# Kernel optimization log

Hardware: AMD Instinct MI355X
Metric: run time of the kernel (lower is better)

The kernel has to match this reference:

```python
import jax, jax.numpy as jnp
import numpy as np

B, S, D_IN, M, H, F, L, D_OUT = 4, 1024, 256, 1024, 16, 8, 2, 256
HD = M // H
EPS = 1e-5


def setup_inputs() -> dict:
    key = jax.random.key(0)
    ks = iter(jax.random.split(key, 40))
    w = lambda *s: 0.02 * jax.random.normal(next(ks), s, dtype=jnp.float32)
    inp = {
        "x": jax.random.normal(next(ks), (B, S, D_IN), dtype=jnp.float32),
        # phase embedding params
        "Wemb": w(D_IN, M), "bemb": w(M),
        "Wamp": w(M, F), "bamp": w(F),
        "freqs": jnp.logspace(-1, 2, F, dtype=jnp.float32),
        "phase_off": w(F),
        # per-layer attention params, stacked on leading L axis
        "Wq": w(L, M, M), "bq": w(L, M),
        "Wk": w(L, M, M), "bk": w(L, M),
        "Wv": w(L, M, M), "bv": w(L, M),
        "Wo": w(L, M, M), "bo": w(L, M),
        "pbias": w(L, H, F),
        "ln_g": jnp.ones((L, M), dtype=jnp.float32),
        "ln_b": jnp.zeros((L, M), dtype=jnp.float32),
        # output projection MLP
        "W1": w(M, M // 2), "b1": w(M // 2),
        "W2": w(M // 2, D_OUT), "b2": w(D_OUT),
    }
    return inp


def _forward(x, Wemb, bemb, Wamp, bamp, freqs, phase_off,
             Wq, bq, Wk, bk, Wv, bv, Wo, bo, pbias, ln_g, ln_b,
             W1, b1, W2, b2):
    Bsz, Seq, _ = x.shape
    # --- TemporalPhaseEmbedding ---
    m = x @ Wemb + bemb                                   # [B,S,M]
    tc = jnp.arange(Seq, dtype=x.dtype) / Seq * (2.0 * jnp.pi)  # [S]
    amp = jax.nn.softmax(m @ Wamp + bamp, axis=-1)        # [B,S,F]
    pc = tc[:, None] * freqs[None, :] + phase_off         # [S,F] (batch-identical)
    # |m[...,None] * amp * e^{i*pc}| averaged over F == |m| * mean_F(amp)
    pf = jnp.abs(m) * jnp.mean(amp, axis=-1, keepdims=True)  # [B,S,M]
    # phase-coherence, batch-independent since pc is shared across batch
    coh = jnp.cos(pc[:, None, :] - pc[None, :, :])        # [S,S,F]
    scale = 1.0 / jnp.sqrt(jnp.asarray(HD, dtype=x.dtype))
    for l in range(L):
        res = pf
        Q = (pf @ Wq[l] + bq[l]).reshape(Bsz, Seq, H, HD)
        K = (pf @ Wk[l] + bk[l]).reshape(Bsz, Seq, H, HD)
        V = (pf @ Wv[l] + bv[l]).reshape(Bsz, Seq, H, HD)
        bias = jnp.einsum('stf,hf->hst', coh, pbias[l])   # [H,S,S]
        scores = jnp.einsum('bshd,bthd->bhst', Q, K) * scale + bias[None]
        w_attn = jax.nn.softmax(scores, axis=-1)
        att = jnp.einsum('bhst,bthd->bshd', w_attn, V).reshape(Bsz, Seq, M)
        att = att @ Wo[l] + bo[l]
        y = att + res
        mu = jnp.mean(y, axis=-1, keepdims=True)
        var = jnp.var(y, axis=-1, keepdims=True)
        pf = (y - mu) / jnp.sqrt(var + EPS) * ln_g[l] + ln_b[l]
    hdn = jax.nn.relu(pf @ W1 + b1)
    return hdn @ W2 + b2                                  # [B,S,D_OUT]


def reference(x, Wemb, bemb, Wamp, bamp, freqs, phase_off,
              Wq, bq, Wk, bk, Wv, bv, Wo, bo, pbias, ln_g, ln_b,
              W1, b1, W2, b2):
    return _forward(x, Wemb, bemb, Wamp, bamp, freqs, phase_off,
                    Wq, bq, Wk, bk, Wv, bv, Wo, bo, pbias, ln_g, ln_b,
                    W1, b1, W2, b2)
```

## Files before the change

### kernel.cpp

```cpp
#include <hip/hip_runtime.h>
#include <cmath>

#define B_    4
#define S_    1024
#define DIN_  256
#define M_    1024
#define H_    16
#define F_    8
#define L_    2
#define DOUT_ 256
#define NT_   4096

typedef unsigned short u16;
typedef unsigned int   u32;
typedef __bf16 bf16x8 __attribute__((ext_vector_type(8)));
typedef float  f32x4  __attribute__((ext_vector_type(4)));

#define LOG2E 1.4426950408889634f
#define QSCALE (0.125f * LOG2E)

__device__ __forceinline__ u16 f2b(float f) {
    u32 u = __builtin_bit_cast(u32, f);
    u += 0x7fffu + ((u >> 16) & 1u);
    return (u16)(u >> 16);
}
__device__ __forceinline__ float b2f(u32 h) {
    return __builtin_bit_cast(float, h << 16);
}
__device__ __forceinline__ void gload_lds16(const void* g, void* l) {
    __builtin_amdgcn_global_load_lds(
        (const __attribute__((address_space(1))) u32*)g,
        (__attribute__((address_space(3))) u32*)l, 16, 0, 0);
}

__global__ void qcsb_k(const float* __restrict__ freqs,
                       const float* __restrict__ poff,
                       const float* __restrict__ pb,
                       u16* __restrict__ qcs, u16* __restrict__ csb)
{
    const int QN = L_ * H_ * S_ * 16;
    int idx = blockIdx.x * 256 + threadIdx.x;
    if (idx < QN) {
        int f2 = idx & 15, f = f2 & 7;
        int s = (idx >> 4) & 1023;
        int lh = idx >> 14;
        float pc = ((float)s * (6.283185307179586f / 1024.f)) * freqs[f] + poff[f];
        float v = (f2 < 8) ? cosf(pc) : sinf(pc);
        qcs[idx] = f2b(pb[lh * 8 + f] * v * LOG2E);
    } else if (idx < QN + S_ * 16) {
        int i2 = idx - QN;
        int f2 = i2 & 15, f = f2 & 7;
        int s = i2 >> 4;
        float pc = ((float)s * (6.283185307179586f / 1024.f)) * freqs[f] + poff[f];
        csb[i2] = f2b((f2 < 8) ? cosf(pc) : sinf(pc));
    }
}

__global__ void bcat_k(const float* __restrict__ bq, const float* __restrict__ bk,
                       const float* __restrict__ bv, float* __restrict__ bqkv)
{
    int idx = blockIdx.x * 256 + threadIdx.x;
    int l = idx >= 3072;
    int j = idx - l * 3072;
    float v = (j < 1024) ? bq[l * 1024 + j]
            : (j < 2048) ? bk[l * 1024 + j - 1024]
                         : bv[l * 1024 + j - 2048];
    bqkv[idx] = v;
}

__global__ __launch_bounds__(256) void cvt_k(const float* __restrict__ src,
                                             u16* __restrict__ dst)
{
    int i = (blockIdx.x * 256 + threadIdx.x) * 4;
    float4 v = *(const float4*)(src + i);
    *(ushort4*)(dst + i) = make_ushort4(f2b(v.x), f2b(v.y), f2b(v.z), f2b(v.w));
}

__global__ __launch_bounds__(256) void cvtT_k(const float* __restrict__ src,
                                              u16* __restrict__ dst, int K, int N)
{
    __shared__ float t[32][33];
    src += (size_t)blockIdx.z * K * N;
    dst += (size_t)blockIdx.z * K * N;
    const int n0 = blockIdx.x * 32, k0 = blockIdx.y * 32;
    const int r = threadIdx.x >> 3, c4 = (threadIdx.x & 7) << 2;
    float4 v = *(const float4*)(src + (size_t)(k0 + r) * N + n0 + c4);
    t[r][c4 + 0] = v.x; t[r][c4 + 1] = v.y; t[r][c4 + 2] = v.z; t[r][c4 + 3] = v.w;
    __syncthreads();
    ushort4 o = make_ushort4(f2b(t[c4 + 0][r]), f2b(t[c4 + 1][r]),
                             f2b(t[c4 + 2][r]), f2b(t[c4 + 3][r]));
    *(ushort4*)(dst + (size_t)(n0 + r) * K + k0 + c4) = o;
}

__global__ __launch_bounds__(256) void cvtT3_k(const float* __restrict__ Wq,
                                               const float* __restrict__ Wk,
                                               const float* __restrict__ Wv,
                                               u16* __restrict__ dst)
{
    __shared__ float t[32][33];
    const int z = blockIdx.z, l = z / 3, which = z - l * 3;
    const float* src = (which == 0 ? Wq : which == 1 ? Wk : Wv) + (size_t)l * M_ * M_;
    u16* d = dst + (size_t)l * 3072 * 1024 + (size_t)which * 1024 * 1024;
    const int n0 = blockIdx.x * 32, k0 = blockIdx.y * 32;
    const int r = threadIdx.x >> 3, c4 = (threadIdx.x & 7) << 2;
    float4 v = *(const float4*)(src + (size_t)(k0 + r) * 1024 + n0 + c4);
    t[r][c4 + 0] = v.x; t[r][c4 + 1] = v.y; t[r][c4 + 2] = v.z; t[r][c4 + 3] = v.w;
    __syncthreads();
    ushort4 o = make_ushort4(f2b(t[c4 + 0][r]), f2b(t[c4 + 1][r]),
                             f2b(t[c4 + 2][r]), f2b(t[c4 + 3][r]));
    *(ushort4*)(d + (size_t)(n0 + r) * 1024 + k0 + c4) = o;
}

__global__ __launch_bounds__(256) void vT_k(const u16* __restrict__ QKV,
                                            u16* __restrict__ Vt)
{
    __shared__ __attribute__((aligned(16))) u16 Ts[64 * 64];
    const int tid = threadIdx.x;
    const int t0 = blockIdx.x * 64, bh = blockIdx.y;
    const int b = bh >> 4, h = bh & 15;
#pragma unroll
    for (int i = 0; i < 2; ++i) {
        int slot = i * 256 + tid;
        int row = slot >> 3, g8 = slot & 7;
        uint4 v = *(const uint4*)(QKV + (size_t)(b * 1024 + t0 + row) * 3072 + 2048 + h * 64 + g8 * 8);
        int gs = g8 ^ ((row >> 3) & 7);
        *(uint4*)(Ts + row * 64 + gs * 8) = v;
    }
    __syncthreads();
#pragma unroll
    for (int i = 0; i < 2; ++i) {
        int slot = i * 256 + tid;
        int d = slot >> 3, t8 = slot & 7;
        u16 tmp[8];
#pragma unroll
        for (int j = 0; j < 8; ++j) {
            int t = t8 * 8 + j;
            int gd = (d >> 3) ^ ((t >> 3) & 7);
            tmp[j] = Ts[t * 64 + gd * 8 + (d & 7)];
        }
        *(uint4*)(Vt + (size_t)(bh * 64 + d) * 1024 + t0 + t8 * 8) = *(uint4*)tmp;
    }
}

template<int EPI, int OUTBF>
__global__ __launch_bounds__(256, 2) void mgemm_k(
    const u16* __restrict__ A, const u16* __restrict__ Wt,
    const float* __restrict__ bias, void* __restrict__ Cout,
    int N, int K)
{
    __shared__ __attribute__((aligned(16))) u16 As[128 * 64];
    __shared__ __attribute__((aligned(16))) u16 Bs[128 * 64];
    const int tid = threadIdx.x;
    const int lane = tid & 63;
    const int bn = blockIdx.x, bm = blockIdx.y;
    const int wid = tid >> 6, wr = wid >> 1, wc = wid & 1;

    f32x4 acc[4][4];
#pragma unroll
    for (int m = 0; m < 4; ++m)
#pragma unroll
        for (int n = 0; n < 4; ++n) {
            f32x4 z = {0.f, 0.f, 0.f, 0.f};
            acc[m][n] = z;
        }

    const int r = lane & 15, g = lane >> 4;
    const int nk = K >> 6;

    for (int kt = 0; kt < nk; ++kt) {
        const int k0 = kt << 6;
        __syncthreads();
#pragma unroll
        for (int i = 0; i < 4; ++i) {
            int slot = i * 256 + tid;
            int row = slot >> 3;
            int kg = (slot & 7) ^ (row & 7);
            gload_lds16(A + (size_t)(bm * 128 + row) * K + k0 + kg * 8,
                        As + (size_t)(slot & ~63) * 8);
        }
#pragma unroll
        for (int i = 0; i < 4; ++i) {
            int slot = i * 256 + tid;
            int row = slot >> 3;
            int kg = (slot & 7) ^ (row & 7);
            gload_lds16(Wt + (size_t)(bn * 128 + row) * K + k0 + kg * 8,
                        Bs + (size_t)(slot & ~63) * 8);
        }
        __syncthreads();

#pragma unroll
        for (int ks = 0; ks < 2; ++ks) {
            bf16x8 af[4], bfr[4];
#pragma unroll
            for (int m = 0; m < 4; ++m) {
                int row = wr * 64 + m * 16 + r;
                int kg = (ks * 4 + g) ^ (row & 7);
                af[m] = *(const bf16x8*)(As + row * 64 + kg * 8);
            }
#pragma unroll
            for (int n = 0; n < 4; ++n) {
                int row = wc * 64 + n * 16 + r;
                int kg = (ks * 4 + g) ^ (row & 7);
                bfr[n] = *(const bf16x8*)(Bs + row * 64 + kg * 8);
            }
#pragma unroll
            for (int m = 0; m < 4; ++m)
#pragma unroll
                for (int n = 0; n < 4; ++n)
                    acc[m][n] = __builtin_amdgcn_mfma_f32_16x16x32_bf16(
                        af[m], bfr[n], acc[m][n], 0, 0, 0);
        }
    }

#pragma unroll
    for (int n = 0; n < 4; ++n) {
        const int gcol = bn * 128 + wc * 64 + n * 16 + r;
        const float bb = bias[gcol];
#pragma unroll
        for (int m = 0; m < 4; ++m) {
            const int grow0 = bm * 128 + wr * 64 + m * 16 + g * 4;
#pragma unroll
            for (int q = 0; q < 4; ++q) {
                float c = acc[m][n][q] + bb;
                if (EPI == 1) c = fabsf(c) * 0.125f;
                if (EPI == 2) c = fmaxf(c, 0.f);
                if (EPI == 4) c = (gcol < 1024) ? c * QSCALE : c;
                if (OUTBF)
                    ((u16*)Cout)[(size_t)(grow0 + q) * N + gcol] = f2b(c);
                else
                    ((float*)Cout)[(size_t)(grow0 + q) * N + gcol] = c;
            }
        }
    }
}

__global__ __launch_bounds__(512) void fattn_k(
    const u16* __restrict__ QKV, const u16* __restrict__ Vtg,
    const u16* __restrict__ csb, const u16* __restrict__ qcs,
    u16* __restrict__ Og)
{
    __shared__ __attribute__((aligned(16))) u16 Ks2[64 * 64];
    __shared__ __attribute__((aligned(16))) u16 Vt2[64 * 64];
    __shared__ __attribute__((aligned(16))) u16 Ext[64 * 16];
    __shared__ __attribute__((aligned(16))) u16 Pl[8][16 * 68];
    const int tid = threadIdx.x, lane = tid & 63, w = tid >> 6;
    const int c = lane & 15, g = lane >> 4;
    const int h = blockIdx.y, b = blockIdx.z, bh = b * 16 + h;
    const int s0 = blockIdx.x * 128;

    const uint4 zz = {0u, 0u, 0u, 0u};
    const bf16x8 zfrag = __builtin_bit_cast(bf16x8, zz);

    bf16x8 aq[3];
    {
        int sl = s0 + w * 16 + c;
        size_t tok = (size_t)b * 1024 + sl;
        aq[0] = *(const bf16x8*)(QKV + tok * 3072 + h * 64 + g * 8);
        aq[1] = *(const bf16x8*)(QKV + tok * 3072 + h * 64 + 32 + g * 8);
        aq[2] = (g < 2) ? *(const bf16x8*)(qcs + ((size_t)h * 1024 + sl) * 16 + g * 8)
                        : zfrag;
    }

    f32x4 oacc[4];
#pragma unroll
    for (int n = 0; n < 4; ++n) {
        f32x4 z = {0.f, 0.f, 0.f, 0.f};
        oacc[n] = z;
    }
    float lsum = 0.f;

    for (int t0 = 0; t0 < S_; t0 += 64) {
        __syncthreads();
        {
            int row = tid >> 3, gi = tid & 7;
            int kg = (gi ^ (row & 7)) * 8;
            gload_lds16(QKV + (size_t)(b * 1024 + t0 + row) * 3072 + 1024 + h * 64 + kg,
                        Ks2 + (size_t)(tid & ~63) * 8);
            gload_lds16(Vtg + (size_t)(bh * 64 + row) * 1024 + t0 + kg,
                        Vt2 + (size_t)(tid & ~63) * 8);
        }
        if (tid < 128) {
            int row = tid >> 1, gi = tid & 1;
            gload_lds16(csb + (size_t)(t0 + row) * 16 + gi * 8,
                        Ext + (size_t)(tid & ~63) * 8);
        }
        __syncthreads();

        f32x4 sacc[4];
#pragma unroll
        for (int n = 0; n < 4; ++n) {
            f32x4 z = {0.f, 0.f, 0.f, 0.f};
            sacc[n] = z;
        }
#pragma unroll
        for (int ks = 0; ks < 3; ++ks) {
            bf16x8 bk[4];
#pragma unroll
            for (int n = 0; n < 4; ++n) {
                int tr = n * 16 + c;
                if (ks < 2) {
                    int kg = (ks * 4 + g) ^ (tr & 7);
                    bk[n] = *(const bf16x8*)(Ks2 + tr * 64 + kg * 8);
                } else {
                    bk[n] = (g < 2) ? *(const bf16x8*)(Ext + tr * 16 + g * 8) : zfrag;
                }
            }
#pragma unroll
            for (int n = 0; n < 4; ++n)
                sacc[n] = __builtin_amdgcn_mfma_f32_16x16x32_bf16(
                    bk[n], aq[ks], sacc[n], 0, 0, 0);
        }

#pragma unroll
        for (int n = 0; n < 4; ++n) {
            u16 pk[4];
#pragma unroll
            for (int q = 0; q < 4; ++q) {
                float p = __builtin_amdgcn_exp2f(sacc[n][q]);
                lsum += p;
                pk[q] = f2b(p);
            }
            uint2 pv;
            pv.x = (u32)pk[0] | ((u32)pk[1] << 16);
            pv.y = (u32)pk[2] | ((u32)pk[3] << 16);
            *(uint2*)(&Pl[w][c * 68 + n * 16 + g * 4]) = pv;
        }

#pragma unroll
        for (int ks2 = 0; ks2 < 2; ++ks2) {
            bf16x8 pa = *(const bf16x8*)(&Pl[w][c * 68 + ks2 * 32 + g * 8]);
#pragma unroll
            for (int n = 0; n < 4; ++n) {
                int dr = n * 16 + c;
                int kg = (ks2 * 4 + g) ^ (dr & 7);
                bf16x8 vf = *(const bf16x8*)(Vt2 + dr * 64 + kg * 8);
                oacc[n] = __builtin_amdgcn_mfma_f32_16x16x32_bf16(
                    pa, vf, oacc[n], 0, 0, 0);
            }
        }
    }

    float lt = lsum + __shfl_xor(lsum, 16);
    lt += __shfl_xor(lt, 32);
    float inv[4];
#pragma unroll
    for (int q = 0; q < 4; ++q)
        inv[q] = 1.f / __shfl(lt, g * 4 + q);

#pragma unroll
    for (int n = 0; n < 4; ++n)
#pragma unroll
        for (int q = 0; q < 4; ++q) {
            size_t tok = (size_t)b * 1024 + s0 + w * 16 + g * 4 + q;
            Og[tok * 1024 + h * 64 + n * 16 + c] = f2b(oacc[n][q] * inv[q]);
        }
}

__global__ __launch_bounds__(256) void ln_k(
    const u16* __restrict__ Y, u16* __restrict__ Pf,
    const float* __restrict__ g, const float* __restrict__ bt)
{
    const int rw = blockIdx.x;
    const int tid = threadIdx.x;
    const u16* yp = Y + (size_t)rw * M_ + tid * 4;
    u16* pp = Pf + (size_t)rw * M_ + tid * 4;
    ushort4 yv = *(const ushort4*)yp;
    ushort4 rv = *(const ushort4*)pp;
    float a[4];
    a[0] = b2f(yv.x) + b2f(rv.x); a[1] = b2f(yv.y) + b2f(rv.y);
    a[2] = b2f(yv.z) + b2f(rv.z); a[3] = b2f(yv.w) + b2f(rv.w);
    float s = a[0] + a[1] + a[2] + a[3];
    float q = a[0] * a[0] + a[1] * a[1] + a[2] * a[2] + a[3] * a[3];
#pragma unroll
    for (int o = 1; o < 64; o <<= 1) {
        s += __shfl_xor(s, o);
        q += __shfl_xor(q, o);
    }
    __shared__ float ss[4], qq[4];
    if ((tid & 63) == 0) { ss[tid >> 6] = s; qq[tid >> 6] = q; }
    __syncthreads();
    s = ss[0] + ss[1] + ss[2] + ss[3];
    q = qq[0] + qq[1] + qq[2] + qq[3];
    float mu = s * (1.0f / 1024.0f);
    float var = q * (1.0f / 1024.0f) - mu * mu;
    float inv = rsqrtf(var + 1e-5f);
    float4 gv = *(const float4*)(g + (tid << 2));
    float4 bv = *(const float4*)(bt + (tid << 2));
    *(ushort4*)pp = make_ushort4(
        f2b((a[0] - mu) * inv * gv.x + bv.x),
        f2b((a[1] - mu) * inv * gv.y + bv.y),
        f2b((a[2] - mu) * inv * gv.z + bv.z),
        f2b((a[3] - mu) * inv * gv.w + bv.w));
}

extern "C" void kernel_launch(void* const* d_in, const int* in_sizes, int n_in,
                              void* d_out, int out_size, void* d_ws, size_t ws_size,
                              hipStream_t stream)
{
    const float* x     = (const float*)d_in[0];
    const float* Wemb  = (const float*)d_in[1];
    const float* bemb  = (const float*)d_in[2];
    const float* freqs = (const float*)d_in[5];
    const float* poff  = (const float*)d_in[6];
    const float* Wq    = (const float*)d_in[7];
    const float* bq    = (const float*)d_in[8];
    const float* Wk    = (const float*)d_in[9];
    const float* bk    = (const float*)d_in[10];
    const float* Wv    = (const float*)d_in[11];
    const float* bv    = (const float*)d_in[12];
    const float* Wo    = (const float*)d_in[13];
    const float* bo    = (const float*)d_in[14];
    const float* pbias = (const float*)d_in[15];
    const float* lng   = (const float*)d_in[16];
    const float* lnb   = (const float*)d_in[17];
    const float* W1    = (const float*)d_in[18];
    const float* b1    = (const float*)d_in[19];
    const float* W2    = (const float*)d_in[20];
    const float* b2    = (const float*)d_in[21];
    float* out = (float*)d_out;

    char* ws = (char*)d_ws;
    const size_t MB = 1 << 20;
    u16* pf    = (u16*)(ws);
    u16* QKV   = (u16*)(ws + 8 * MB);
    u16* Ab    = (u16*)(ws + 32 * MB);
    u16* Vtg   = (u16*)(ws + 40 * MB);
    u16* WqkvT = (u16*)(ws + 48 * MB);
    u16* WoT   = (u16*)(ws + 60 * MB);
    u16* WembT = (u16*)(ws + 64 * MB);
    u16* W1T   = (u16*)(ws + 64 * MB + 512 * 1024);
    u16* W2T   = (u16*)(ws + 65 * MB + 512 * 1024);
    u16* xb    = (u16*)(ws + 66 * MB);
    u16* qcs   = (u16*)(ws + 68 * MB);
    u16* csb   = (u16*)(ws + 69 * MB);
    float* bqkv = (float*)(ws + 69 * MB + 64 * 1024);

    dim3 blk(256);
    cvt_k<<<1024, blk, 0, stream>>>(x, xb);
    cvtT3_k<<<dim3(32, 32, 6), blk, 0, stream>>>(Wq, Wk, Wv, WqkvT);
    cvtT_k<<<dim3(32, 32, 2), blk, 0, stream>>>(Wo, WoT, 1024, 1024);
    cvtT_k<<<dim3(32, 8, 1), blk, 0, stream>>>(Wemb, WembT, 256, 1024);
    cvtT_k<<<dim3(16, 32, 1), blk, 0, stream>>>(W1, W1T, 1024, 512);
    cvtT_k<<<dim3(8, 16, 1), blk, 0, stream>>>(W2, W2T, 512, 256);
    qcsb_k<<<2112, blk, 0, stream>>>(freqs, poff, pbias, qcs, csb);
    bcat_k<<<24, blk, 0, stream>>>(bq, bk, bv, bqkv);

    mgemm_k<1, 1><<<dim3(8, 32), blk, 0, stream>>>(xb, WembT, bemb, pf, 1024, 256);

    for (int l = 0; l < L_; ++l) {
        mgemm_k<4, 1><<<dim3(24, 32), blk, 0, stream>>>(
            pf, WqkvT + (size_t)l * 3072 * 1024, bqkv + l * 3072, QKV, 3072, 1024);
        vT_k<<<dim3(16, 64), blk, 0, stream>>>(QKV, Vtg);
        fattn_k<<<dim3(8, 16, 4), dim3(512), 0, stream>>>(
            QKV, Vtg, csb, qcs + (size_t)l * H_ * S_ * 16, Ab);
        mgemm_k<0, 1><<<dim3(8, 32), blk, 0, stream>>>(
            Ab, WoT + (size_t)l * M_ * M_, bo + l * M_, QKV , 1024, 1024);
        ln_k<<<dim3(NT_), blk, 0, stream>>>(QKV, pf, lng + l * M_, lnb + l * M_);
    }

    mgemm_k<2, 1><<<dim3(4, 32), blk, 0, stream>>>(pf, W1T, b1, Ab, 512, 1024);
    mgemm_k<0, 0><<<dim3(2, 32), blk, 0, stream>>>(Ab, W2T, b2, out, 256, 512);
}
```

Before: 263.6 us.

## Fuse V transpose into QKV GEMM epilogue and double-buffer attention K/V tiles

The QKV projection GEMM now writes the V columns directly in transposed per-head layout, so the separate vT_k kernel and its extra read and write of V go away. The flash-attention kernel double-buffers its K, V and phase-bias tiles in LDS, prefetching the next tile while computing the current one. It waits on partial vmcnt and uses raw barriers with setprio around the MFMA sections. This adds LDS use and relies on hand-counted vmcnt values that must match the number of outstanding loads per wave.

```diff
diff --git a/kernel.cpp b/kernel.cpp
--- a/kernel.cpp
+++ b/kernel.cpp
@@ -111,42 +111,11 @@
     *(ushort4*)(d + (size_t)(n0 + r) * 1024 + k0 + c4) = o;
 }
 
-__global__ __launch_bounds__(256) void vT_k(const u16* __restrict__ QKV,
-                                            u16* __restrict__ Vt)
-{
-    __shared__ __attribute__((aligned(16))) u16 Ts[64 * 64];
-    const int tid = threadIdx.x;
-    const int t0 = blockIdx.x * 64, bh = blockIdx.y;
-    const int b = bh >> 4, h = bh & 15;
-#pragma unroll
-    for (int i = 0; i < 2; ++i) {
-        int slot = i * 256 + tid;
-        int row = slot >> 3, g8 = slot & 7;
-        uint4 v = *(const uint4*)(QKV + (size_t)(b * 1024 + t0 + row) * 3072 + 2048 + h * 64 + g8 * 8);
-        int gs = g8 ^ ((row >> 3) & 7);
-        *(uint4*)(Ts + row * 64 + gs * 8) = v;
-    }
-    __syncthreads();
-#pragma unroll
-    for (int i = 0; i < 2; ++i) {
-        int slot = i * 256 + tid;
-        int d = slot >> 3, t8 = slot & 7;
-        u16 tmp[8];
-#pragma unroll
-        for (int j = 0; j < 8; ++j) {
-            int t = t8 * 8 + j;
-            int gd = (d >> 3) ^ ((t >> 3) & 7);
-            tmp[j] = Ts[t * 64 + gd * 8 + (d & 7)];
-        }
-        *(uint4*)(Vt + (size_t)(bh * 64 + d) * 1024 + t0 + t8 * 8) = *(uint4*)tmp;
-    }
-}
-
 template<int EPI, int OUTBF>
 __global__ __launch_bounds__(256, 2) void mgemm_k(
     const u16* __restrict__ A, const u16* __restrict__ Wt,
     const float* __restrict__ bias, void* __restrict__ Cout,
-    int N, int K)
+    u16* __restrict__ vt, int N, int K)
 {
     __shared__ __attribute__((aligned(16))) u16 As[128 * 64];
     __shared__ __attribute__((aligned(16))) u16 Bs[128 * 64];
@@ -219,16 +188,28 @@
 #pragma unroll
         for (int m = 0; m < 4; ++m) {
             const int grow0 = bm * 128 + wr * 64 + m * 16 + g * 4;
-#pragma unroll
-            for (int q = 0; q < 4; ++q) {
-                float c = acc[m][n][q] + bb;
-                if (EPI == 1) c = fabsf(c) * 0.125f;
-                if (EPI == 2) c = fmaxf(c, 0.f);
-                if (EPI == 4) c = (gcol < 1024) ? c * QSCALE : c;
-                if (OUTBF)
-                    ((u16*)Cout)[(size_t)(grow0 + q) * N + gcol] = f2b(c);
-                else
-                    ((float*)Cout)[(size_t)(grow0 + q) * N + gcol] = c;
+            if (EPI == 5 && gcol >= 2048) {
+                int d = gcol - 2048;
+                int bh = (grow0 >> 10) * 16 + (d >> 6);
+                u16 pk[4];
+#pragma unroll
+                for (int q = 0; q < 4; ++q) pk[q] = f2b(acc[m][n][q] + bb);
+                uint2 pv;
+                pv.x = (u32)pk[0] | ((u32)pk[1] << 16);
+                pv.y = (u32)pk[2] | ((u32)pk[3] << 16);
+                *(uint2*)(vt + ((size_t)bh * 64 + (d & 63)) * 1024 + (grow0 & 1023)) = pv;
+            } else {
+#pragma unroll
+                for (int q = 0; q < 4; ++q) {
+                    float c = acc[m][n][q] + bb;
+                    if (EPI == 1) c = fabsf(c) * 0.125f;
+                    if (EPI == 2) c = fmaxf(c, 0.f);
+                    if (EPI == 5) c = (gcol < 1024) ? c * QSCALE : c;
+                    if (OUTBF)
+                        ((u16*)Cout)[(size_t)(grow0 + q) * N + gcol] = f2b(c);
+                    else
+                        ((float*)Cout)[(size_t)(grow0 + q) * N + gcol] = c;
+                }
             }
         }
     }
@@ -239,9 +220,9 @@
     const u16* __restrict__ csb, const u16* __restrict__ qcs,
     u16* __restrict__ Og)
 {
-    __shared__ __attribute__((aligned(16))) u16 Ks2[64 * 64];
-    __shared__ __attribute__((aligned(16))) u16 Vt2[64 * 64];
-    __shared__ __attribute__((aligned(16))) u16 Ext[64 * 16];
+    __shared__ __attribute__((aligned(16))) u16 Ks2[2][64 * 64];
+    __shared__ __attribute__((aligned(16))) u16 Vt2[2][64 * 64];
+    __shared__ __attribute__((aligned(16))) u16 Ext[2][64 * 16];
     __shared__ __attribute__((aligned(16))) u16 Pl[8][16 * 68];
     const int tid = threadIdx.x, lane = tid & 63, w = tid >> 6;
     const int c = lane & 15, g = lane >> 4;
@@ -269,22 +250,35 @@
     }
     float lsum = 0.f;
 
-    for (int t0 = 0; t0 < S_; t0 += 64) {
-        __syncthreads();
-        {
-            int row = tid >> 3, gi = tid & 7;
-            int kg = (gi ^ (row & 7)) * 8;
-            gload_lds16(QKV + (size_t)(b * 1024 + t0 + row) * 3072 + 1024 + h * 64 + kg,
-                        Ks2 + (size_t)(tid & ~63) * 8);
-            gload_lds16(Vtg + (size_t)(bh * 64 + row) * 1024 + t0 + kg,
-                        Vt2 + (size_t)(tid & ~63) * 8);
-        }
+    auto STAGE = [&](int buf, int t0) {
+        int row = tid >> 3, gi = tid & 7;
+        int kg = (gi ^ (row & 7)) * 8;
+        gload_lds16(QKV + (size_t)(b * 1024 + t0 + row) * 3072 + 1024 + h * 64 + kg,
+                    &Ks2[buf][(size_t)(tid & ~63) * 8]);
+        gload_lds16(Vtg + (size_t)(bh * 64 + row) * 1024 + t0 + kg,
+                    &Vt2[buf][(size_t)(tid & ~63) * 8]);
         if (tid < 128) {
-            int row = tid >> 1, gi = tid & 1;
-            gload_lds16(csb + (size_t)(t0 + row) * 16 + gi * 8,
-                        Ext + (size_t)(tid & ~63) * 8);
-        }
-        __syncthreads();
+            int r2 = tid >> 1, g2 = tid & 1;
+            gload_lds16(csb + (size_t)(t0 + r2) * 16 + g2 * 8,
+                        &Ext[buf][(size_t)(tid & ~63) * 8]);
+        }
+    };
+
+    STAGE(0, 0);
+    __builtin_amdgcn_sched_barrier(0);
+
+    for (int it = 0; it < 16; ++it) {
+        const int cur = it & 1;
+        if (it < 15) {
+            STAGE(cur ^ 1, (it + 1) << 6);
+            if (w < 2) asm volatile("s_waitcnt vmcnt(3)" ::: "memory");
+            else       asm volatile("s_waitcnt vmcnt(2)" ::: "memory");
+        } else {
+            asm volatile("s_waitcnt vmcnt(0)" ::: "memory");
+        }
+        __builtin_amdgcn_sched_barrier(0);
+        __builtin_amdgcn_s_barrier();
+        __builtin_amdgcn_sched_barrier(0);
 
         f32x4 sacc[4];
 #pragma unroll
@@ -292,6 +286,7 @@
             f32x4 z = {0.f, 0.f, 0.f, 0.f};
             sacc[n] = z;
         }
+        __builtin_amdgcn_s_setprio(1);
 #pragma unroll
         for (int ks = 0; ks < 3; ++ks) {
             bf16x8 bk[4];
@@ -300,9 +295,9 @@
                 int tr = n * 16 + c;
                 if (ks < 2) {
                     int kg = (ks * 4 + g) ^ (tr & 7);
-                    bk[n] = *(const bf16x8*)(Ks2 + tr * 64 + kg * 8);
+                    bk[n] = *(const bf16x8*)(&Ks2[cur][tr * 64 + kg * 8]);
                 } else {
-                    bk[n] = (g < 2) ? *(const bf16x8*)(Ext + tr * 16 + g * 8) : zfrag;
+                    bk[n] = (g < 2) ? *(const bf16x8*)(&Ext[cur][tr * 16 + g * 8]) : zfrag;
                 }
             }
 #pragma unroll
@@ -310,6 +305,7 @@
                 sacc[n] = __builtin_amdgcn_mfma_f32_16x16x32_bf16(
                     bk[n], aq[ks], sacc[n], 0, 0, 0);
         }
+        __builtin_amdgcn_s_setprio(0);
 
 #pragma unroll
         for (int n = 0; n < 4; ++n) {
@@ -326,6 +322,7 @@
             *(uint2*)(&Pl[w][c * 68 + n * 16 + g * 4]) = pv;
         }
 
+        __builtin_amdgcn_s_setprio(1);
 #pragma unroll
         for (int ks2 = 0; ks2 < 2; ++ks2) {
             bf16x8 pa = *(const bf16x8*)(&Pl[w][c * 68 + ks2 * 32 + g * 8]);
@@ -333,11 +330,16 @@
             for (int n = 0; n < 4; ++n) {
                 int dr = n * 16 + c;
                 int kg = (ks2 * 4 + g) ^ (dr & 7);
-                bf16x8 vf = *(const bf16x8*)(Vt2 + dr * 64 + kg * 8);
+                bf16x8 vf = *(const bf16x8*)(&Vt2[cur][dr * 64 + kg * 8]);
                 oacc[n] = __builtin_amdgcn_mfma_f32_16x16x32_bf16(
                     pa, vf, oacc[n], 0, 0, 0);
             }
         }
+        __builtin_amdgcn_s_setprio(0);
+
+        __builtin_amdgcn_sched_barrier(0);
+        __builtin_amdgcn_s_barrier();
+        __builtin_amdgcn_sched_barrier(0);
     }
 
     float lt = lsum + __shfl_xor(lsum, 16);
@@ -445,19 +447,18 @@
     qcsb_k<<<2112, blk, 0, stream>>>(freqs, poff, pbias, qcs, csb);
     bcat_k<<<24, blk, 0, stream>>>(bq, bk, bv, bqkv);
 
-    mgemm_k<1, 1><<<dim3(8, 32), blk, 0, stream>>>(xb, WembT, bemb, pf, 1024, 256);
+    mgemm_k<1, 1><<<dim3(8, 32), blk, 0, stream>>>(xb, WembT, bemb, pf, nullptr, 1024, 256);
 
     for (int l = 0; l < L_; ++l) {
-        mgemm_k<4, 1><<<dim3(24, 32), blk, 0, stream>>>(
-            pf, WqkvT + (size_t)l * 3072 * 1024, bqkv + l * 3072, QKV, 3072, 1024);
-        vT_k<<<dim3(16, 64), blk, 0, stream>>>(QKV, Vtg);
+        mgemm_k<5, 1><<<dim3(24, 32), blk, 0, stream>>>(
+            pf, WqkvT + (size_t)l * 3072 * 1024, bqkv + l * 3072, QKV, Vtg, 3072, 1024);
         fattn_k<<<dim3(8, 16, 4), dim3(512), 0, stream>>>(
             QKV, Vtg, csb, qcs + (size_t)l * H_ * S_ * 16, Ab);
         mgemm_k<0, 1><<<dim3(8, 32), blk, 0, stream>>>(
-            Ab, WoT + (size_t)l * M_ * M_, bo + l * M_, QKV , 1024, 1024);
+            Ab, WoT + (size_t)l * M_ * M_, bo + l * M_, QKV , nullptr, 1024, 1024);
         ln_k<<<dim3(NT_), blk, 0, stream>>>(QKV, pf, lng + l * M_, lnb + l * M_);
     }
 
-    mgemm_k<2, 1><<<dim3(4, 32), blk, 0, stream>>>(pf, W1T, b1, Ab, 512, 1024);
-    mgemm_k<0, 0><<<dim3(2, 32), blk, 0, stream>>>(Ab, W2T, b2, out, 256, 512);
-}
+    mgemm_k<2, 1><<<dim3(4, 32), blk, 0, stream>>>(pf, W1T, b1, Ab, nullptr, 512, 1024);
+    mgemm_k<0, 0><<<dim3(2, 32), blk, 0, stream>>>(Ab, W2T, b2, out, nullptr, 256, 512);
+}
```

Result: no change. 259.5 us (-1.5%).
